# Kernel optimization log

Hardware: AMD Instinct MI355X
Metric: run time of the kernel (lower is better)

Reference implementation:

```python
import jax, jax.numpy as jnp
import numpy as np

N_NODES = 100000
NNZ_FEAT = 2000000
N_EDGES = 1600000
IN_DIM = 256
OUT_DIM = 64
KEEP_PROB = 0.9  # 1 - dropout(0.1)


def spmm(rows, cols, vals, dense, n_rows):
    # (sparse COO [n_rows, k]) @ dense [k, d] -> [n_rows, d]
    contrib = vals[:, None] * dense[cols]          # [nnz, d] gather
    return jax.ops.segment_sum(contrib, rows, num_segments=n_rows)


def setup_inputs() -> dict:
    key = jax.random.key(0)
    ks = jax.random.split(key, 8)
    x_rows = jax.random.randint(ks[0], (NNZ_FEAT,), 0, N_NODES)
    x_cols = jax.random.randint(ks[1], (NNZ_FEAT,), 0, IN_DIM)
    x_values = jax.random.normal(ks[2], (NNZ_FEAT,), dtype=jnp.float32)
    adj_rows = jax.random.randint(ks[3], (N_EDGES,), 0, N_NODES)
    adj_cols = jax.random.randint(ks[4], (N_EDGES,), 0, N_NODES)
    adj_values = jax.random.uniform(ks[5], (N_EDGES,), dtype=jnp.float32)
    drop_uniform = jax.random.uniform(ks[6], (NNZ_FEAT,), dtype=jnp.float32)
    weights = jax.random.normal(ks[7], (IN_DIM, OUT_DIM), dtype=jnp.float32) * (1.0 / np.sqrt(IN_DIM))
    return {
        "x_rows": x_rows, "x_cols": x_cols, "x_values": x_values,
        "adj_rows": adj_rows, "adj_cols": adj_cols, "adj_values": adj_values,
        "drop_uniform": drop_uniform, "weights": weights,
    }


def reference(x_rows, x_cols, x_values, adj_rows, adj_cols, adj_values, drop_uniform, weights):
    # DropoutSparse: keep entry iff floor(keep_prob + u) == 1, i.e. u >= 1-keep_prob;
    # kept values scaled by 1/keep_prob. Zeroing dropped values == removing them for SpMM.
    keep = jnp.floor(KEEP_PROB + drop_uniform) >= 1.0
    vals = jnp.where(keep, x_values * (1.0 / KEEP_PROB), 0.0)
    h = spmm(x_rows, x_cols, vals, weights, N_NODES)        # [N, OUT_DIM] = X @ W
    out = spmm(adj_rows, adj_cols, adj_values, h, N_NODES)  # [N, OUT_DIM] = A @ (XW)
    return jax.nn.relu(out)
```

## Files before the change

kernel.cpp:

```cpp
#include <hip/hip_runtime.h>

#define N_NODES  100000
#define NNZ_FEAT 2000000
#define N_EDGES  1600000
#define IN_DIM   256
#define OUT_DIM  64

__device__ __forceinline__ bool keep_entry(float u) {
    return floorf(0.9f + u) >= 1.0f;
}


__global__ void hist_fused(const int* __restrict__ xr, const float* __restrict__ du,
                           const int* __restrict__ ar,
                           int* __restrict__ cnt_x, int* __restrict__ cnt_a,
                           int* __restrict__ offs_x, int* __restrict__ offs_a) {
    int i = blockIdx.x * blockDim.x + threadIdx.x;
    if (i < NNZ_FEAT) {
        if (keep_entry(du[i])) {
            offs_x[i] = atomicAdd(&cnt_x[xr[i]], 1);
        }
    } else {
        int e = i - NNZ_FEAT;
        if (e < N_EDGES) {
            offs_a[e] = atomicAdd(&cnt_a[ar[e]], 1);
        }
    }
}

__global__ void scan_pass1(const int* __restrict__ cntX, const int* __restrict__ cntA,
                           int* __restrict__ exX, int* __restrict__ exA,
                           int* __restrict__ bsX, int* __restrict__ bsA, int n) {
    const int* cnt = blockIdx.y ? cntA : cntX;
    int* excl = blockIdx.y ? exA : exX;
    int* bsum = blockIdx.y ? bsA : bsX;
    __shared__ int sh[256];
    int t = threadIdx.x;
    int base = blockIdx.x * 1024 + t * 4;
    int v0 = (base + 0 < n) ? cnt[base + 0] : 0;
    int v1 = (base + 1 < n) ? cnt[base + 1] : 0;
    int v2 = (base + 2 < n) ? cnt[base + 2] : 0;
    int v3 = (base + 3 < n) ? cnt[base + 3] : 0;
    int tsum = v0 + v1 + v2 + v3;
    sh[t] = tsum;
    __syncthreads();
    for (int off = 1; off < 256; off <<= 1) {
        int x = (t >= off) ? sh[t - off] : 0;
        __syncthreads();
        sh[t] += x;
        __syncthreads();
    }
    int texcl = sh[t] - tsum;
    if (base + 0 < n) excl[base + 0] = texcl;
    if (base + 1 < n) excl[base + 1] = texcl + v0;
    if (base + 2 < n) excl[base + 2] = texcl + v0 + v1;
    if (base + 3 < n) excl[base + 3] = texcl + v0 + v1 + v2;
    if (t == 255) bsum[blockIdx.x] = sh[255];
}

__global__ void scan_pass2(const int* __restrict__ bsX, const int* __restrict__ bsA,
                           int* __restrict__ bsSX, int* __restrict__ bsSA,
                           int* __restrict__ totX, int* __restrict__ totA, int nb) {
    const int* bsum = blockIdx.y ? bsA : bsX;
    int* bsumS = blockIdx.y ? bsSA : bsSX;
    int* total = blockIdx.y ? totA : totX;
    __shared__ int sh[128];
    int t = threadIdx.x;
    sh[t] = (t < nb) ? bsum[t] : 0;
    __syncthreads();
    int orig = sh[t];
    for (int off = 1; off < 128; off <<= 1) {
        int x = (t >= off) ? sh[t - off] : 0;
        __syncthreads();
        sh[t] += x;
        __syncthreads();
    }
    if (t < nb) bsumS[t] = sh[t] - orig;
    if (t == 127) *total = sh[127];
}

__global__ void scan_pass3(int* __restrict__ stX, int* __restrict__ stA,
                           const int* __restrict__ bsSX, const int* __restrict__ bsSA,
                           int n) {
    int* startArr = blockIdx.y ? stA : stX;
    const int* bS = blockIdx.y ? bsSA : bsSX;
    int i = blockIdx.x * blockDim.x + threadIdx.x;
    if (i < n) startArr[i] += bS[i >> 10];
}

__global__ void scatter_fused(const int* __restrict__ xr, const int* __restrict__ xc,
                              const float* __restrict__ xv, const float* __restrict__ du,
                              const int* __restrict__ ar, const int* __restrict__ ac,
                              const float* __restrict__ av,
                              const int* __restrict__ startX, const int* __restrict__ startA,
                              const int* __restrict__ offs_x, const int* __restrict__ offs_a,
                              int2* __restrict__ pkX, int2* __restrict__ pkA) {
    const float SCL = (float)(1.0 / 0.9);
    int i = blockIdx.x * blockDim.x + threadIdx.x;
    if (i < NNZ_FEAT) {
        if (!keep_entry(du[i])) return;
        int pos = startX[xr[i]] + offs_x[i];
        pkX[pos] = make_int2(__float_as_int(xv[i] * SCL), xc[i]);
    } else {
        int e = i - NNZ_FEAT;
        if (e < N_EDGES) {
            int pos = startA[ar[e]] + offs_a[e];
            pkA[pos] = make_int2(__float_as_int(av[e]), ac[e]);
        }
    }
}


__global__ void __launch_bounds__(256) spmm1_csr(
        const int* __restrict__ startArr, const int2* __restrict__ pk,
        const float* __restrict__ W, float* __restrict__ h) {
    int wid  = (blockIdx.x * blockDim.x + threadIdx.x) >> 6;
    int lane = threadIdx.x & 63;
    if (wid >= N_NODES) return;
    int s = startArr[wid], e = startArr[wid + 1];
    float acc = 0.0f;
    int j = s;
    for (; j + 8 <= e; j += 8) {
        int2 p0 = pk[j + 0]; int2 p1 = pk[j + 1];
        int2 p2 = pk[j + 2]; int2 p3 = pk[j + 3];
        int2 p4 = pk[j + 4]; int2 p5 = pk[j + 5];
        int2 p6 = pk[j + 6]; int2 p7 = pk[j + 7];
        float g0 = W[p0.y * OUT_DIM + lane];
        float g1 = W[p1.y * OUT_DIM + lane];
        float g2 = W[p2.y * OUT_DIM + lane];
        float g3 = W[p3.y * OUT_DIM + lane];
        float g4 = W[p4.y * OUT_DIM + lane];
        float g5 = W[p5.y * OUT_DIM + lane];
        float g6 = W[p6.y * OUT_DIM + lane];
        float g7 = W[p7.y * OUT_DIM + lane];
        acc = fmaf(__int_as_float(p0.x), g0, acc);
        acc = fmaf(__int_as_float(p1.x), g1, acc);
        acc = fmaf(__int_as_float(p2.x), g2, acc);
        acc = fmaf(__int_as_float(p3.x), g3, acc);
        acc = fmaf(__int_as_float(p4.x), g4, acc);
        acc = fmaf(__int_as_float(p5.x), g5, acc);
        acc = fmaf(__int_as_float(p6.x), g6, acc);
        acc = fmaf(__int_as_float(p7.x), g7, acc);
    }
    if (j + 4 <= e) {
        int2 p0 = pk[j + 0]; int2 p1 = pk[j + 1];
        int2 p2 = pk[j + 2]; int2 p3 = pk[j + 3];
        float g0 = W[p0.y * OUT_DIM + lane];
        float g1 = W[p1.y * OUT_DIM + lane];
        float g2 = W[p2.y * OUT_DIM + lane];
        float g3 = W[p3.y * OUT_DIM + lane];
        acc = fmaf(__int_as_float(p0.x), g0, acc);
        acc = fmaf(__int_as_float(p1.x), g1, acc);
        acc = fmaf(__int_as_float(p2.x), g2, acc);
        acc = fmaf(__int_as_float(p3.x), g3, acc);
        j += 4;
    }
    if (j + 2 <= e) {
        int2 p0 = pk[j + 0]; int2 p1 = pk[j + 1];
        float g0 = W[p0.y * OUT_DIM + lane];
        float g1 = W[p1.y * OUT_DIM + lane];
        acc = fmaf(__int_as_float(p0.x), g0, acc);
        acc = fmaf(__int_as_float(p1.x), g1, acc);
        j += 2;
    }
    if (j < e) {
        int2 p = pk[j];
        acc = fmaf(__int_as_float(p.x), W[p.y * OUT_DIM + lane], acc);
    }
    h[wid * OUT_DIM + lane] = acc;
}

__global__ void __launch_bounds__(256) spmm2_csr(
        const int* __restrict__ startArr, const int2* __restrict__ pk,
        const float* __restrict__ h, float* __restrict__ out) {
    int wid  = (blockIdx.x * blockDim.x + threadIdx.x) >> 6;
    int lane = threadIdx.x & 63;
    if (wid >= N_NODES) return;
    int s = startArr[wid], e = startArr[wid + 1];
    float acc = 0.0f;
    int j = s;
    for (; j + 8 <= e; j += 8) {
        int2 p0 = pk[j + 0]; int2 p1 = pk[j + 1];
        int2 p2 = pk[j + 2]; int2 p3 = pk[j + 3];
        int2 p4 = pk[j + 4]; int2 p5 = pk[j + 5];
        int2 p6 = pk[j + 6]; int2 p7 = pk[j + 7];
        float g0 = h[p0.y * OUT_DIM + lane];
        float g1 = h[p1.y * OUT_DIM + lane];
        float g2 = h[p2.y * OUT_DIM + lane];
        float g3 = h[p3.y * OUT_DIM + lane];
        float g4 = h[p4.y * OUT_DIM + lane];
        float g5 = h[p5.y * OUT_DIM + lane];
        float g6 = h[p6.y * OUT_DIM + lane];
        float g7 = h[p7.y * OUT_DIM + lane];
        acc = fmaf(__int_as_float(p0.x), g0, acc);
        acc = fmaf(__int_as_float(p1.x), g1, acc);
        acc = fmaf(__int_as_float(p2.x), g2, acc);
        acc = fmaf(__int_as_float(p3.x), g3, acc);
        acc = fmaf(__int_as_float(p4.x), g4, acc);
        acc = fmaf(__int_as_float(p5.x), g5, acc);
        acc = fmaf(__int_as_float(p6.x), g6, acc);
        acc = fmaf(__int_as_float(p7.x), g7, acc);
    }
    if (j + 4 <= e) {
        int2 p0 = pk[j + 0]; int2 p1 = pk[j + 1];
        int2 p2 = pk[j + 2]; int2 p3 = pk[j + 3];
        float g0 = h[p0.y * OUT_DIM + lane];
        float g1 = h[p1.y * OUT_DIM + lane];
        float g2 = h[p2.y * OUT_DIM + lane];
        float g3 = h[p3.y * OUT_DIM + lane];
        acc = fmaf(__int_as_float(p0.x), g0, acc);
        acc = fmaf(__int_as_float(p1.x), g1, acc);
        acc = fmaf(__int_as_float(p2.x), g2, acc);
        acc = fmaf(__int_as_float(p3.x), g3, acc);
        j += 4;
    }
    if (j + 2 <= e) {
        int2 p0 = pk[j + 0]; int2 p1 = pk[j + 1];
        float g0 = h[p0.y * OUT_DIM + lane];
        float g1 = h[p1.y * OUT_DIM + lane];
        acc = fmaf(__int_as_float(p0.x), g0, acc);
        acc = fmaf(__int_as_float(p1.x), g1, acc);
        j += 2;
    }
    if (j < e) {
        int2 p = pk[j];
        acc = fmaf(__int_as_float(p.x), h[p.y * OUT_DIM + lane], acc);
    }
    out[wid * OUT_DIM + lane] = fmaxf(acc, 0.0f);
}


extern "C" void kernel_launch(void* const* d_in, const int* in_sizes, int n_in,
                              void* d_out, int out_size, void* d_ws, size_t ws_size,
                              hipStream_t stream) {
    const int*   x_rows       = (const int*)d_in[0];
    const int*   x_cols       = (const int*)d_in[1];
    const float* x_values     = (const float*)d_in[2];
    const int*   adj_rows     = (const int*)d_in[3];
    const int*   adj_cols     = (const int*)d_in[4];
    const float* adj_values   = (const float*)d_in[5];
    const float* drop_uniform = (const float*)d_in[6];
    const float* weights      = (const float*)d_in[7];
    float* out = (float*)d_out;

    char* base = (char*)d_ws;
    size_t off = 0;
    auto carve = [&](size_t bytes) -> void* {
        void* p = base + off;
        off += (bytes + 255) & ~(size_t)255;
        return p;
    };
    float* h       = (float*)carve((size_t)N_NODES * OUT_DIM * sizeof(float));
    int*   cnt_x   = (int*)carve(2 * N_NODES * sizeof(int));
    int*   cnt_a   = cnt_x + N_NODES;
    int*   start_x = (int*)carve((N_NODES + 1) * sizeof(int));
    int*   start_a = (int*)carve((N_NODES + 1) * sizeof(int));
    int*   bsum_x  = (int*)carve(128 * sizeof(int));
    int*   bsumS_x = (int*)carve(128 * sizeof(int));
    int*   bsum_a  = (int*)carve(128 * sizeof(int));
    int*   bsumS_a = (int*)carve(128 * sizeof(int));
    int*   offs_x  = (int*)carve((size_t)NNZ_FEAT * sizeof(int));
    int*   offs_a  = (int*)carve((size_t)N_EDGES * sizeof(int));
    int2*  pk_x    = (int2*)carve((size_t)NNZ_FEAT * sizeof(int2));
    int2*  pk_a    = (int2*)carve((size_t)N_EDGES * sizeof(int2));
    (void)ws_size;

    const int NB = (N_NODES + 1023) / 1024;

    hipMemsetAsync(cnt_x, 0, 2 * N_NODES * sizeof(int), stream);

    {
        int total = NNZ_FEAT + N_EDGES;
        hist_fused<<<(total + 255) / 256, 256, 0, stream>>>(
            x_rows, drop_uniform, adj_rows, cnt_x, cnt_a, offs_x, offs_a);
    }

    scan_pass1<<<dim3(NB, 2), 256, 0, stream>>>(
        cnt_x, cnt_a, start_x, start_a, bsum_x, bsum_a, N_NODES);
    scan_pass2<<<dim3(1, 2), 128, 0, stream>>>(
        bsum_x, bsum_a, bsumS_x, bsumS_a, start_x + N_NODES, start_a + N_NODES, NB);
    scan_pass3<<<dim3((N_NODES + 255) / 256, 2), 256, 0, stream>>>(
        start_x, start_a, bsumS_x, bsumS_a, N_NODES);

    {
        int total = NNZ_FEAT + N_EDGES;
        scatter_fused<<<(total + 255) / 256, 256, 0, stream>>>(
            x_rows, x_cols, x_values, drop_uniform, adj_rows, adj_cols, adj_values,
            start_x, start_a, offs_x, offs_a, pk_x, pk_a);
    }

    {
        long long threads = (long long)N_NODES * OUT_DIM;
        spmm1_csr<<<(unsigned)((threads + 255) / 256), 256, 0, stream>>>(
            start_x, pk_x, weights, h);
        spmm2_csr<<<(unsigned)((threads + 255) / 256), 256, 0, stream>>>(
            start_a, pk_a, h, out);
    }
}
```

Before: 439.4 us.

## Densify sparse features and replace first SpMM with LDS-tiled dense GEMM

Scatters the kept, rescaled feature nonzeros into a dense N x IN_DIM buffer with float atomics, then computes X@W with a dense GEMM that keeps W in shared memory. This removes the CSR build (histogram, scan, scatter) for the feature matrix and the gather-based first SpMM. In exchange it needs a large zeroed workspace and streams about 100 MB for the memset and the GEMM read. It falls back to the old path if the workspace is too small.

Measured after the change: 592.3 us. +34.8%, slower.

```diff
diff --git a/kernel.cpp b/kernel.cpp
--- a/kernel.cpp
+++ b/kernel.cpp
@@ -11,22 +11,76 @@
 }
 
 
-__global__ void hist_fused(const int* __restrict__ xr, const float* __restrict__ du,
-                           const int* __restrict__ ar,
-                           int* __restrict__ cnt_x, int* __restrict__ cnt_a,
-                           int* __restrict__ offs_x, int* __restrict__ offs_a) {
+__global__ void hist_dens(const int* __restrict__ ar,
+                          int* __restrict__ cnt_a, int* __restrict__ offs_a,
+                          const int* __restrict__ xr, const int* __restrict__ xc,
+                          const float* __restrict__ xv, const float* __restrict__ du,
+                          float* __restrict__ Xd) {
     int i = blockIdx.x * blockDim.x + threadIdx.x;
-    if (i < NNZ_FEAT) {
-        if (keep_entry(du[i])) {
-            offs_x[i] = atomicAdd(&cnt_x[xr[i]], 1);
-        }
+    if (i < N_EDGES) {
+        offs_a[i] = atomicAdd(&cnt_a[ar[i]], 1);
     } else {
-        int e = i - NNZ_FEAT;
-        if (e < N_EDGES) {
-            offs_a[e] = atomicAdd(&cnt_a[ar[e]], 1);
-        }
-    }
-}
+        int j = i - N_EDGES;
+        if (j < NNZ_FEAT && keep_entry(du[j])) {
+            unsafeAtomicAdd(&Xd[(size_t)xr[j] * IN_DIM + xc[j]],
+                            xv[j] * (float)(1.0 / 0.9));
+        }
+    }
+}
+
+__global__ void scatter_a(const int* __restrict__ ar, const int* __restrict__ ac,
+                          const float* __restrict__ av,
+                          const int* __restrict__ startA, const int* __restrict__ offs_a,
+                          int2* __restrict__ pkA) {
+    int e = blockIdx.x * blockDim.x + threadIdx.x;
+    if (e < N_EDGES) {
+        int pos = startA[ar[e]] + offs_a[e];
+        pkA[pos] = make_int2(__float_as_int(av[e]), ac[e]);
+    }
+}
+
+__global__ void __launch_bounds__(256) gemm1(const float* __restrict__ Xd,
+                                             const float* __restrict__ W,
+                                             float* __restrict__ h) {
+    __shared__ float Wl[IN_DIM * OUT_DIM];
+    for (int i = threadIdx.x; i < IN_DIM * OUT_DIM / 4; i += 256)
+        ((float4*)Wl)[i] = ((const float4*)W)[i];
+    __syncthreads();
+
+    int wave = threadIdx.x >> 6;
+    int lane = threadIdx.x & 63;
+    for (int g = blockIdx.x; g < N_NODES / 16; g += gridDim.x) {
+        int r0 = g * 16 + wave * 4;
+        const float* x0 = Xd + (size_t)(r0 + 0) * IN_DIM;
+        const float* x1 = Xd + (size_t)(r0 + 1) * IN_DIM;
+        const float* x2 = Xd + (size_t)(r0 + 2) * IN_DIM;
+        const float* x3 = Xd + (size_t)(r0 + 3) * IN_DIM;
+        float a0 = 0.f, a1 = 0.f, a2 = 0.f, a3 = 0.f;
+        for (int k = 0; k < IN_DIM; k += 4) {
+            float4 v0 = *(const float4*)(x0 + k);
+            float4 v1 = *(const float4*)(x1 + k);
+            float4 v2 = *(const float4*)(x2 + k);
+            float4 v3 = *(const float4*)(x3 + k);
+            float w0 = Wl[(k + 0) * OUT_DIM + lane];
+            float w1 = Wl[(k + 1) * OUT_DIM + lane];
+            float w2 = Wl[(k + 2) * OUT_DIM + lane];
+            float w3 = Wl[(k + 3) * OUT_DIM + lane];
+            a0 = fmaf(v0.x, w0, a0); a0 = fmaf(v0.y, w1, a0);
+            a0 = fmaf(v0.z, w2, a0); a0 = fmaf(v0.w, w3, a0);
+            a1 = fmaf(v1.x, w0, a1); a1 = fmaf(v1.y, w1, a1);
+            a1 = fmaf(v1.z, w2, a1); a1 = fmaf(v1.w, w3, a1);
+            a2 = fmaf(v2.x, w0, a2); a2 = fmaf(v2.y, w1, a2);
+            a2 = fmaf(v2.z, w2, a2); a2 = fmaf(v2.w, w3, a2);
+            a3 = fmaf(v3.x, w0, a3); a3 = fmaf(v3.y, w1, a3);
+            a3 = fmaf(v3.z, w2, a3); a3 = fmaf(v3.w, w3, a3);
+        }
+        h[(size_t)(r0 + 0) * OUT_DIM + lane] = a0;
+        h[(size_t)(r0 + 1) * OUT_DIM + lane] = a1;
+        h[(size_t)(r0 + 2) * OUT_DIM + lane] = a2;
+        h[(size_t)(r0 + 3) * OUT_DIM + lane] = a3;
+    }
+}
+
 
 __global__ void scan_pass1(const int* __restrict__ cntX, const int* __restrict__ cntA,
                            int* __restrict__ exX, int* __restrict__ exA,
@@ -88,6 +142,24 @@
     if (i < n) startArr[i] += bS[i >> 10];
 }
 
+
+__global__ void hist_fused(const int* __restrict__ xr, const float* __restrict__ du,
+                           const int* __restrict__ ar,
+                           int* __restrict__ cnt_x, int* __restrict__ cnt_a,
+                           int* __restrict__ offs_x, int* __restrict__ offs_a) {
+    int i = blockIdx.x * blockDim.x + threadIdx.x;
+    if (i < NNZ_FEAT) {
+        if (keep_entry(du[i])) {
+            offs_x[i] = atomicAdd(&cnt_x[xr[i]], 1);
+        }
+    } else {
+        int e = i - NNZ_FEAT;
+        if (e < N_EDGES) {
+            offs_a[e] = atomicAdd(&cnt_a[ar[e]], 1);
+        }
+    }
+}
+
 __global__ void scatter_fused(const int* __restrict__ xr, const int* __restrict__ xc,
                               const float* __restrict__ xv, const float* __restrict__ du,
                               const int* __restrict__ ar, const int* __restrict__ ac,
@@ -110,7 +182,6 @@
     }
 }
 
-
 __global__ void __launch_bounds__(256) spmm1_csr(
         const int* __restrict__ startArr, const int2* __restrict__ pk,
         const float* __restrict__ W, float* __restrict__ h) {
@@ -243,6 +314,8 @@
     const float* weights      = (const float*)d_in[7];
     float* out = (float*)d_out;
 
+    const int NB = (N_NODES + 1023) / 1024;
+
     char* base = (char*)d_ws;
     size_t off = 0;
     auto carve = [&](size_t bytes) -> void* {
@@ -251,49 +324,83 @@
         return p;
     };
     float* h       = (float*)carve((size_t)N_NODES * OUT_DIM * sizeof(float));
+    float* Xd      = (float*)carve((size_t)N_NODES * IN_DIM * sizeof(float));
+    int*   cnt_a   = (int*)carve(N_NODES * sizeof(int));
+    int*   start_a = (int*)carve((N_NODES + 1) * sizeof(int));
+    int*   bsum_a  = (int*)carve(128 * sizeof(int));
+    int*   bsumS_a = (int*)carve(128 * sizeof(int));
+    int*   offs_a  = (int*)carve((size_t)N_EDGES * sizeof(int));
+    int2*  pk_a    = (int2*)carve((size_t)N_EDGES * sizeof(int2));
+    size_t needed_main = off;
+
+    if (ws_size >= needed_main) {
+        hipMemsetAsync(cnt_a, 0, N_NODES * sizeof(int), stream);
+        hipMemsetAsync(Xd, 0, (size_t)N_NODES * IN_DIM * sizeof(float), stream);
+
+        {
+            int total = N_EDGES + NNZ_FEAT;
+            hist_dens<<<(total + 255) / 256, 256, 0, stream>>>(
+                adj_rows, cnt_a, offs_a, x_rows, x_cols, x_values, drop_uniform, Xd);
+        }
+
+        scan_pass1<<<dim3(NB, 1), 256, 0, stream>>>(
+            cnt_a, nullptr, start_a, nullptr, bsum_a, nullptr, N_NODES);
+        scan_pass2<<<dim3(1, 1), 128, 0, stream>>>(
+            bsum_a, nullptr, bsumS_a, nullptr, start_a + N_NODES, nullptr, NB);
+        scan_pass3<<<dim3((N_NODES + 255) / 256, 1), 256, 0, stream>>>(
+            start_a, nullptr, bsumS_a, nullptr, N_NODES);
+
+        scatter_a<<<(N_EDGES + 255) / 256, 256, 0, stream>>>(
+            adj_rows, adj_cols, adj_values, start_a, offs_a, pk_a);
+
+        gemm1<<<2048, 256, 0, stream>>>(Xd, weights, h);
+
+        {
+            long long threads = (long long)N_NODES * OUT_DIM;
+            spmm2_csr<<<(unsigned)((threads + 255) / 256), 256, 0, stream>>>(
+                start_a, pk_a, h, out);
+        }
+        return;
+    }
+
+    off = 0;
+    float* fh      = (float*)carve((size_t)N_NODES * OUT_DIM * sizeof(float));
     int*   cnt_x   = (int*)carve(2 * N_NODES * sizeof(int));
-    int*   cnt_a   = cnt_x + N_NODES;
+    int*   cnt_a2  = cnt_x + N_NODES;
     int*   start_x = (int*)carve((N_NODES + 1) * sizeof(int));
-    int*   start_a = (int*)carve((N_NODES + 1) * sizeof(int));
+    int*   start_a2= (int*)carve((N_NODES + 1) * sizeof(int));
     int*   bsum_x  = (int*)carve(128 * sizeof(int));
     int*   bsumS_x = (int*)carve(128 * sizeof(int));
-    int*   bsum_a  = (int*)carve(128 * sizeof(int));
-    int*   bsumS_a = (int*)carve(128 * sizeof(int));
+    int*   bsum_a2 = (int*)carve(128 * sizeof(int));
+    int*   bsumS_a2= (int*)carve(128 * sizeof(int));
     int*   offs_x  = (int*)carve((size_t)NNZ_FEAT * sizeof(int));
-    int*   offs_a  = (int*)carve((size_t)N_EDGES * sizeof(int));
+    int*   offs_a2 = (int*)carve((size_t)N_EDGES * sizeof(int));
     int2*  pk_x    = (int2*)carve((size_t)NNZ_FEAT * sizeof(int2));
-    int2*  pk_a    = (int2*)carve((size_t)N_EDGES * sizeof(int2));
-    (void)ws_size;
-
-    const int NB = (N_NODES + 1023) / 1024;
+    int2*  pk_a2   = (int2*)carve((size_t)N_EDGES * sizeof(int2));
 
     hipMemsetAsync(cnt_x, 0, 2 * N_NODES * sizeof(int), stream);
-
     {
         int total = NNZ_FEAT + N_EDGES;
         hist_fused<<<(total + 255) / 256, 256, 0, stream>>>(
-            x_rows, drop_uniform, adj_rows, cnt_x, cnt_a, offs_x, offs_a);
-    }
-
+            x_rows, drop_uniform, adj_rows, cnt_x, cnt_a2, offs_x, offs_a2);
+    }
     scan_pass1<<<dim3(NB, 2), 256, 0, stream>>>(
-        cnt_x, cnt_a, start_x, start_a, bsum_x, bsum_a, N_NODES);
+        cnt_x, cnt_a2, start_x, start_a2, bsum_x, bsum_a2, N_NODES);
     scan_pass2<<<dim3(1, 2), 128, 0, stream>>>(
-        bsum_x, bsum_a, bsumS_x, bsumS_a, start_x + N_NODES, start_a + N_NODES, NB);
+        bsum_x, bsum_a2, bsumS_x, bsumS_a2, start_x + N_NODES, start_a2 + N_NODES, NB);
     scan_pass3<<<dim3((N_NODES + 255) / 256, 2), 256, 0, stream>>>(
-        start_x, start_a, bsumS_x, bsumS_a, N_NODES);
-
+        start_x, start_a2, bsumS_x, bsumS_a2, N_NODES);
     {
         int total = NNZ_FEAT + N_EDGES;
         scatter_fused<<<(total + 255) / 256, 256, 0, stream>>>(
             x_rows, x_cols, x_values, drop_uniform, adj_rows, adj_cols, adj_values,
-            start_x, start_a, offs_x, offs_a, pk_x, pk_a);
-    }
-
+            start_x, start_a2, offs_x, offs_a2, pk_x, pk_a2);
+    }
     {
         long long threads = (long long)N_NODES * OUT_DIM;
         spmm1_csr<<<(unsigned)((threads + 255) / 256), 256, 0, stream>>>(
-            start_x, pk_x, weights, h);
+            start_x, pk_x, weights, fh);
         spmm2_csr<<<(unsigned)((threads + 255) / 256), 256, 0, stream>>>(
-            start_a, pk_a, h, out);
-    }
-}
+            start_a2, pk_a2, fh, out);
+    }
+}
```
